# Kernel optimization log

Measured on AMD Instinct MI355X. Metric: run time of the kernel, lower is better.

The kernel has to match this reference:

```python
import jax, jax.numpy as jnp
import numpy as np

PROBE = 1.0
ALPHA = 0.5


def setup_inputs() -> dict:
    key = jax.random.key(0)
    ks = jax.random.split(key, 8)
    B, L, D = 4096, 128, 64  # batch, n_cats (fields), d_embed
    NG, NL = 2, 2
    cat_indices = jax.random.randint(ks[0], (B, L), 0, L, dtype=jnp.int64)
    emb_table = jax.random.normal(ks[1], (L, D), dtype=jnp.float32)
    acc_w = jax.random.normal(ks[2], (D, D), dtype=jnp.float32) * (1.0 / np.sqrt(D))
    acc_b = jnp.zeros((D,), dtype=jnp.float32)
    gw = jax.random.normal(ks[3], (NG, D, D), dtype=jnp.float32) * (1.0 / np.sqrt(D))
    gb = jnp.zeros((NG, D), dtype=jnp.float32)
    lw = jax.random.normal(ks[4], (NL, D, D), dtype=jnp.float32) * (1.0 / np.sqrt(D))
    lb = jnp.zeros((NL, D), dtype=jnp.float32)
    return {"cat_indices": cat_indices, "emb_table": emb_table, "acc_w": acc_w,
            "acc_b": acc_b, "gw": gw, "gb": gb, "lw": lw, "lb": lb}


def reference(cat_indices, emb_table, acc_w, acc_b, gw, gb, lw, lb):
    B, L = cat_indices.shape
    # shallow embedding lookup: [B, L, D]
    emb = emb_table[cat_indices]
    # uniform + probe*I adjacency, row-normalized by (L + probe); identical per sample
    adj = (jnp.ones((L, L), emb.dtype) + PROBE * jnp.eye(L, dtype=emb.dtype)) / (L + PROBE)
    # global branch: adj @ (emb @ W) + b
    support = jnp.einsum('bld,de->ble', emb, acc_w)
    g = jnp.einsum('lm,bme->ble', adj, support) + acc_b
    g = jax.nn.relu(g)
    n_global = gw.shape[0]
    for i in range(n_global):
        g = jnp.einsum('bld,ed->ble', g, gw[i]) + gb[i]
        if i + 1 < n_global:
            g = jax.nn.relu(g)
    # local FM branch: 0.5 * ((sum e)^2 - sum e^2)  -> [B, D]
    s = jnp.sum(emb, axis=1)
    loc = 0.5 * (s * s - jnp.sum(emb * emb, axis=1))
    n_local = lw.shape[0]
    for i in range(n_local):
        loc = loc @ lw[i].T + lb[i]
        if i + 1 < n_local:
            loc = jax.nn.relu(loc)
    # broadcast local [B, D] against global [B, L, D]
    return ALPHA * g + (1.0 - ALPHA) * loc[:, None, :]
```

## Files before the change

kernel.cpp:

```cpp
#include <hip/hip_runtime.h>
#include <hip/hip_bf16.h>


typedef __attribute__((ext_vector_type(8))) short bf16x8;
typedef __attribute__((ext_vector_type(4))) float f32x4;
typedef __attribute__((ext_vector_type(2))) unsigned int u32x2;

#define RECIP129 (1.0f/129.0f)

static __device__ __forceinline__ unsigned int cvt_pk_bf16(float lo, float hi){
  unsigned int r;
  asm("v_cvt_pk_bf16_f32 %0, %1, %2" : "=v"(r) : "v"(lo), "v"(hi));
  return r;
}

__global__ __launch_bounds__(64) void prep_kernel(const float* __restrict__ emb,
                                                  const float* __restrict__ acc_w,
                                                  const float* __restrict__ lw,
                                                  const float* __restrict__ gw,
                                                  unsigned int* __restrict__ tsupb,
                                                  uint4* __restrict__ fragtab){
  const int e = threadIdx.x, blk = blockIdx.x;
  const int r = e & 15, h = e >> 4;
  if (blk < 128){
    float acc = 0.f;
    #pragma unroll
    for (int d = 0; d < 64; ++d) acc += emb[blk*64 + d] * acc_w[d*64 + e];
    acc *= RECIP129;
    float alo = __shfl(acc, 2*(e & 31));
    float ahi = __shfl(acc, 2*(e & 31) + 1);
    if (e < 32) tsupb[blk*32 + e] = cvt_pk_bf16(alo, ahi);
  } else if (blk < 144){
    int f = blk - 128;
    int layer = f >> 3, nt = (f >> 1) & 3, kc = f & 1;
    float sc = layer ? 0.5f : 1.0f;
    const float* p0 = gw + layer*4096 + (nt*16 + r)*64 + kc*32 + h*8;
    float4 a = *reinterpret_cast<const float4*>(p0);
    float4 c = *reinterpret_cast<const float4*>(p0 + 4);
    uint4 v;
    v.x = cvt_pk_bf16(sc*a.x, sc*a.y); v.y = cvt_pk_bf16(sc*a.z, sc*a.w);
    v.z = cvt_pk_bf16(sc*c.x, sc*c.y); v.w = cvt_pk_bf16(sc*c.z, sc*c.w);
    fragtab[f*64 + e] = v;
  } else if (blk < 176){
    int g = blk - 144;
    int sq = g >= 16; if (sq) g -= 16;
    int nt = g >> 2, kc = g & 3;
    const float* base = emb + (kc*32 + h*8)*64 + nt*16 + r;
    unsigned int q[4];
    #pragma unroll
    for (int j2 = 0; j2 < 4; ++j2){
      float x = base[(2*j2)*64], y = base[(2*j2 + 1)*64];
      if (sq){ x *= x; y *= y; }
      q[j2] = cvt_pk_bf16(x, y);
    }
    uint4 v; v.x=q[0]; v.y=q[1]; v.z=q[2]; v.w=q[3];
    fragtab[(16 + sq*16 + g)*64 + e] = v;
  } else if (blk < 184){
    int g = blk - 176;
    int nt = g >> 1, kc = g & 1;
    const float* base = acc_w + (kc*32 + h*8)*64 + nt*16 + r;
    unsigned int q[4];
    #pragma unroll
    for (int j2 = 0; j2 < 4; ++j2)
      q[j2] = cvt_pk_bf16(base[(2*j2)*64]*RECIP129, base[(2*j2+1)*64]*RECIP129);
    uint4 v; v.x=q[0]; v.y=q[1]; v.z=q[2]; v.w=q[3];
    fragtab[(48 + g)*64 + e] = v;
  } else {
    int g = blk - 184;
    int layer = g >> 3, nt = (g >> 1) & 3, kc = g & 1;
    const float* p0 = lw + layer*4096 + (nt*16 + r)*64 + kc*32 + h*8;
    float4 a = *reinterpret_cast<const float4*>(p0);
    float4 c = *reinterpret_cast<const float4*>(p0 + 4);
    uint4 v;
    v.x = cvt_pk_bf16(a.x, a.y); v.y = cvt_pk_bf16(a.z, a.w);
    v.z = cvt_pk_bf16(c.x, c.y); v.w = cvt_pk_bf16(c.z, c.w);
    fragtab[(56 + g)*64 + e] = v;
  }
}

__global__ __launch_bounds__(512) void mega_kernel(
    const int*          __restrict__ cat,
    const unsigned int* __restrict__ tsupb,
    const float*        __restrict__ acc_b,
    const float*        __restrict__ lb,
    const float*        __restrict__ gbias,
    const uint4*        __restrict__ fragtab,
    float*              __restrict__ out)
{
  __shared__ int hist[16*128];
  __shared__ __align__(16) unsigned int  cbf[16*64];
  __shared__ __align__(16) unsigned short srows[16*64];
  __shared__ __align__(16) unsigned short lrows[16*64];
  __shared__ float u_s[16][68];
  __shared__ float l2_s[16][68];
  __shared__ __align__(16) unsigned short ts[128*72];
  __shared__ __align__(16) unsigned short gbuf[8][16*64];

  const int tid = threadIdx.x, w = tid >> 6, lane = tid & 63;
  const int r = lane & 15, h = lane >> 4;
  const int bbase = blockIdx.x * 16;
  const unsigned int swzr = (unsigned)(r & 7) << 4;

  bf16x8 w0[4][2], w1[4][2];
  #pragma unroll
  for (int nt = 0; nt < 4; ++nt)
    #pragma unroll
    for (int kc = 0; kc < 2; ++kc){
      w0[nt][kc] = __builtin_bit_cast(bf16x8, fragtab[(nt*2 + kc)*64 + lane]);
      w1[nt][kc] = __builtin_bit_cast(bf16x8, fragtab[(8 + nt*2 + kc)*64 + lane]);
    }
  f32x4 gb0f[4];
  #pragma unroll
  for (int mt = 0; mt < 4; ++mt){
    float4 gv = *reinterpret_cast<const float4*>(gbias + mt*16 + h*4);
    f32x4 g; g[0]=gv.x; g[1]=gv.y; g[2]=gv.z; g[3]=gv.w;
    gb0f[mt] = g;
  }

  bf16x8 af_s[4], af_q[4], aw[2], l0f[2], l1f[2];
  float accb[4], lb0v[4], bias05[4];
  f32x4 acc_h = {0,0,0,0};
  if (w < 4){
    #pragma unroll
    for (int kc = 0; kc < 4; ++kc){
      af_s[kc] = __builtin_bit_cast(bf16x8, fragtab[(16 + w*4 + kc)*64 + lane]);
      af_q[kc] = __builtin_bit_cast(bf16x8, fragtab[(32 + w*4 + kc)*64 + lane]);
    }
    #pragma unroll
    for (int kc = 0; kc < 2; ++kc){
      aw[kc]  = __builtin_bit_cast(bf16x8, fragtab[(48 + w*2 + kc)*64 + lane]);
      l0f[kc] = __builtin_bit_cast(bf16x8, fragtab[(56 + w*2 + kc)*64 + lane]);
      l1f[kc] = __builtin_bit_cast(bf16x8, fragtab[(64 + w*2 + kc)*64 + lane]);
    }
    const int n = w*16 + h*4;
    #pragma unroll
    for (int reg = 0; reg < 4; ++reg){
      accb[reg]   = acc_b[n + reg];
      lb0v[reg]   = lb[n + reg];
      bias05[reg] = 0.5f*(lb[64 + n + reg] + gbias[64 + n + reg]);
    }
  }

  #pragma unroll
  for (int i = 0; i < 4; ++i) hist[tid*4 + i] = 0;
  __syncthreads();

  if (w < 4){
    int b_l = tid >> 4, l0 = (tid & 15) * 8;
    const int* cp = cat + (bbase + b_l)*128 + l0;
    int4 i0 = *reinterpret_cast<const int4*>(cp);
    int4 i1 = *reinterpret_cast<const int4*>(cp + 4);
    atomicAdd(&hist[b_l*128 + i0.x], 1); atomicAdd(&hist[b_l*128 + i0.y], 1);
    atomicAdd(&hist[b_l*128 + i0.z], 1); atomicAdd(&hist[b_l*128 + i0.w], 1);
    atomicAdd(&hist[b_l*128 + i1.x], 1); atomicAdd(&hist[b_l*128 + i1.y], 1);
    atomicAdd(&hist[b_l*128 + i1.z], 1); atomicAdd(&hist[b_l*128 + i1.w], 1);
  } else {
    int t2 = tid - 256;
    int k = t2 >> 1, half = t2 & 1;
    const uint4* src = reinterpret_cast<const uint4*>(tsupb) + k*8 + half*4;
    char* rowp = (char*)&ts[k*72];
    unsigned int swz = (unsigned)(k & 3) << 4;
    #pragma unroll
    for (int i = 0; i < 4; ++i)
      *reinterpret_cast<uint4*>(rowp + ((unsigned)(half*64 + i*16) ^ swz)) = src[i];
  }
  __syncthreads();

  if (w < 4){
    int b_l = tid >> 4, c0 = (tid & 15) * 8;
    float f[8];
    #pragma unroll
    for (int i = 0; i < 8; ++i) f[i] = (float)hist[b_l*128 + c0 + i];
    uint4 v;
    v.x = cvt_pk_bf16(f[0], f[1]); v.y = cvt_pk_bf16(f[2], f[3]);
    v.z = cvt_pk_bf16(f[4], f[5]); v.w = cvt_pk_bf16(f[6], f[7]);
    *reinterpret_cast<uint4*>((char*)cbf + b_l*256 + ((unsigned)(c0*2) ^ ((unsigned)(b_l & 7) << 4))) = v;
  }
  __syncthreads();

  if (w < 4){
    const char* crow = (const char*)cbf + r*256;
    f32x4 acc_s = {0,0,0,0}, acc_q = {0,0,0,0};
    #pragma unroll
    for (int kc = 0; kc < 4; ++kc){
      bf16x8 cf = __builtin_bit_cast(bf16x8,
          *reinterpret_cast<const uint4*>(crow + ((unsigned)(kc*64 + h*16) ^ swzr)));
      acc_s = __builtin_amdgcn_mfma_f32_16x16x32_bf16(af_s[kc], cf, acc_s, 0, 0, 0);
      acc_q = __builtin_amdgcn_mfma_f32_16x16x32_bf16(af_q[kc], cf, acc_q, 0, 0, 0);
    }
    char* srow = (char*)srows + r*128;
    char* lrow = (char*)lrows + r*128;
    const unsigned int off = ((unsigned)(w*32 + h*8)) ^ swzr;
    u32x2 ps, pl;
    ps[0] = cvt_pk_bf16(acc_s[0], acc_s[1]);
    ps[1] = cvt_pk_bf16(acc_s[2], acc_s[3]);
    float l0 = 0.5f*(acc_s[0]*acc_s[0] - acc_q[0]);
    float l1 = 0.5f*(acc_s[1]*acc_s[1] - acc_q[1]);
    float l2v = 0.5f*(acc_s[2]*acc_s[2] - acc_q[2]);
    float l3 = 0.5f*(acc_s[3]*acc_s[3] - acc_q[3]);
    pl[0] = cvt_pk_bf16(l0, l1); pl[1] = cvt_pk_bf16(l2v, l3);
    *reinterpret_cast<u32x2*>(srow + off) = ps;
    *reinterpret_cast<u32x2*>(lrow + off) = pl;
  }
  __syncthreads();

  if (w < 4){
    f32x4 acc_u; acc_u[0]=accb[0]; acc_u[1]=accb[1]; acc_u[2]=accb[2]; acc_u[3]=accb[3];
    #pragma unroll
    for (int kc = 0; kc < 2; ++kc){
      unsigned o = ((unsigned)(kc*64 + h*16)) ^ swzr;
      bf16x8 sb = __builtin_bit_cast(bf16x8, *reinterpret_cast<const uint4*>((char*)srows + r*128 + o));
      bf16x8 lf = __builtin_bit_cast(bf16x8, *reinterpret_cast<const uint4*>((char*)lrows + r*128 + o));
      acc_u = __builtin_amdgcn_mfma_f32_16x16x32_bf16(aw[kc],  sb, acc_u, 0, 0, 0);
      acc_h = __builtin_amdgcn_mfma_f32_16x16x32_bf16(l0f[kc], lf, acc_h, 0, 0, 0);
    }
    f32x4 st; st[0]=acc_u[0]; st[1]=acc_u[1]; st[2]=acc_u[2]; st[3]=acc_u[3];
    *reinterpret_cast<f32x4*>(&u_s[r][w*16 + h*4]) = st;
  }
  __syncthreads();
  if (w < 4){
    char* lrow = (char*)lrows + r*128;
    const unsigned int off = ((unsigned)(w*32 + h*8)) ^ swzr;
    u32x2 ph;
    ph[0] = cvt_pk_bf16(fmaxf(acc_h[0] + lb0v[0], 0.f), fmaxf(acc_h[1] + lb0v[1], 0.f));
    ph[1] = cvt_pk_bf16(fmaxf(acc_h[2] + lb0v[2], 0.f), fmaxf(acc_h[3] + lb0v[3], 0.f));
    *reinterpret_cast<u32x2*>(lrow + off) = ph;
  }
  __syncthreads();

  if (w < 4){
    f32x4 acc2 = {0,0,0,0};
    #pragma unroll
    for (int kc = 0; kc < 2; ++kc){
      unsigned o = ((unsigned)(kc*64 + h*16)) ^ swzr;
      bf16x8 hf = __builtin_bit_cast(bf16x8, *reinterpret_cast<const uint4*>((char*)lrows + r*128 + o));
      acc2 = __builtin_amdgcn_mfma_f32_16x16x32_bf16(l1f[kc], hf, acc2, 0, 0, 0);
    }
    f32x4 st;
    st[0] = 0.5f*acc2[0] + bias05[0]; st[1] = 0.5f*acc2[1] + bias05[1];
    st[2] = 0.5f*acc2[2] + bias05[2]; st[3] = 0.5f*acc2[3] + bias05[3];
    *reinterpret_cast<f32x4*>(&l2_s[r][w*16 + h*4]) = st;
  }
  __syncthreads();

  char* myrowW = (char*)&gbuf[w][0] + r*128;
  const unsigned int rsw8 = (unsigned)(r & 7) << 4;

  for (int bi = 0; bi < 2; ++bi){
    const int b_l = w*2 + bi;
    const int b = bbase + b_l;
    int ki0 = cat[b*128 + lane];
    int ki1 = cat[b*128 + 64 + lane];

    float uf[16];
    #pragma unroll
    for (int kc = 0; kc < 2; ++kc)
      #pragma unroll
      for (int j = 0; j < 8; ++j)
        uf[kc*8 + j] = u_s[b_l][kc*32 + h*8 + j];

    f32x4 c2i[4];
    #pragma unroll
    for (int mt = 0; mt < 4; ++mt){
      f32x4 t;
      t[0] = l2_s[b_l][mt*16 + h*4 + 0]; t[1] = l2_s[b_l][mt*16 + h*4 + 1];
      t[2] = l2_s[b_l][mt*16 + h*4 + 2]; t[3] = l2_s[b_l][mt*16 + h*4 + 3];
      c2i[mt] = t;
    }

    for (int tl = 0; tl < 8; ++tl){
      const int rowbase = b*128 + tl*16;
      int kk = __shfl(tl < 4 ? ki0 : ki1, (tl & 3)*16 + r);

      const char* trow = (const char*)&ts[kk*72];
      const unsigned int ksw = (unsigned)(kk & 3) << 4;
      bf16x8 a0[2];
      #pragma unroll
      for (int kc = 0; kc < 2; ++kc){
        uint4 wv = *reinterpret_cast<const uint4*>(trow + ((unsigned)(kc*64 + h*16) ^ ksw));
        unsigned int ow[4];
        const unsigned int* wp = &wv.x;
        #pragma unroll
        for (int q = 0; q < 4; ++q){
          unsigned int wq = wp[q];
          float lo = fmaxf(__uint_as_float(wq << 16)         + uf[kc*8 + 2*q],     0.f);
          float hi = fmaxf(__uint_as_float(wq & 0xffff0000u) + uf[kc*8 + 2*q + 1], 0.f);
          ow[q] = cvt_pk_bf16(lo, hi);
        }
        uint4 packed; packed.x=ow[0]; packed.y=ow[1]; packed.z=ow[2]; packed.w=ow[3];
        a0[kc] = __builtin_bit_cast(bf16x8, packed);
      }

      f32x4 acc1[4];
      #pragma unroll
      for (int nt = 0; nt < 4; ++nt) acc1[nt] = gb0f[nt];
      #pragma unroll
      for (int kc = 0; kc < 2; ++kc)
        #pragma unroll
        for (int nt = 0; nt < 4; ++nt)
          acc1[nt] = __builtin_amdgcn_mfma_f32_16x16x32_bf16(w0[nt][kc], a0[kc], acc1[nt], 0, 0, 0);

      #pragma unroll
      for (int nt = 0; nt < 4; ++nt){
        u32x2 p;
        p[0] = cvt_pk_bf16(fmaxf(acc1[nt][0], 0.f), fmaxf(acc1[nt][1], 0.f));
        p[1] = cvt_pk_bf16(fmaxf(acc1[nt][2], 0.f), fmaxf(acc1[nt][3], 0.f));
        *reinterpret_cast<u32x2*>(myrowW + ((unsigned)(nt*32 + h*8) ^ rsw8)) = p;
      }

      bf16x8 a1[2];
      #pragma unroll
      for (int kc = 0; kc < 2; ++kc)
        a1[kc] = __builtin_bit_cast(bf16x8,
                   *reinterpret_cast<const uint4*>(myrowW + ((unsigned)(kc*64 + h*16) ^ rsw8)));

      f32x4 acc2[4];
      #pragma unroll
      for (int mt = 0; mt < 4; ++mt) acc2[mt] = c2i[mt];
      #pragma unroll
      for (int kc = 0; kc < 2; ++kc)
        #pragma unroll
        for (int mt = 0; mt < 4; ++mt)
          acc2[mt] = __builtin_amdgcn_mfma_f32_16x16x32_bf16(w1[mt][kc], a1[kc], acc2[mt], 0, 0, 0);

      float* orow = out + (size_t)(rowbase + r)*64 + h*4;
      #pragma unroll
      for (int mt = 0; mt < 4; ++mt){
        float4 st;
        st.x = acc2[mt][0]; st.y = acc2[mt][1];
        st.z = acc2[mt][2]; st.w = acc2[mt][3];
        *reinterpret_cast<float4*>(orow + mt*16) = st;
      }
    }
  }
}

extern "C" void kernel_launch(void* const* d_in, const int* in_sizes, int n_in,
                              void* d_out, int out_size, void* d_ws, size_t ws_size,
                              hipStream_t stream) {
  const int*   cat   = (const int*)  d_in[0];
  const float* emb   = (const float*)d_in[1];
  const float* acc_w = (const float*)d_in[2];
  const float* acc_b = (const float*)d_in[3];
  const float* gw    = (const float*)d_in[4];
  const float* gb    = (const float*)d_in[5];
  const float* lw    = (const float*)d_in[6];
  const float* lb    = (const float*)d_in[7];
  float* out = (float*)d_out;

  const int B = in_sizes[0] / 128;

  float* ws           = (float*)d_ws;
  unsigned int* tsupb = (unsigned int*)ws;
  uint4* fragtab      = (uint4*)(ws + 4096);

  hipLaunchKernelGGL(prep_kernel, dim3(200), dim3(64), 0, stream,
                     emb, acc_w, lw, gw, tsupb, fragtab);
  hipLaunchKernelGGL(mega_kernel, dim3(B/16), dim3(512), 0, stream,
                     cat, tsupb, acc_b, lb, gb, fragtab, out);
}
```

Before: 37.00 us.

## Halve batch rows per block, add occupancy hint, defer weight loads, nontemporal stores

Each block now handles 8 samples instead of 16, so the grid doubles and each wave processes a single sample instead of looping over two. The histogram build is restructured so every wave reads its own indices once, reusing them for both the atomics and the main loop. The table copy into shared memory is spread across all threads and overlaps with the histogram zeroing, which removes one barrier. Global-branch weight fragments are loaded only after the local phase, to cut register pressure alongside the __launch_bounds__(512,3) hint. Output writes use nontemporal stores. The trade-off is that prep work per block (shared table copy, local MFMAs computed on padded 16-row tiles) is now amortized over half as many samples.

```diff
diff --git a/kernel.cpp b/kernel.cpp
--- a/kernel.cpp
+++ b/kernel.cpp
@@ -78,7 +78,7 @@
   }
 }
 
-__global__ __launch_bounds__(512) void mega_kernel(
+__global__ __launch_bounds__(512, 3) void mega_kernel(
     const int*          __restrict__ cat,
     const unsigned int* __restrict__ tsupb,
     const float*        __restrict__ acc_b,
@@ -87,35 +87,32 @@
     const uint4*        __restrict__ fragtab,
     float*              __restrict__ out)
 {
-  __shared__ int hist[16*128];
+  __shared__ int hist[8*128];
   __shared__ __align__(16) unsigned int  cbf[16*64];
   __shared__ __align__(16) unsigned short srows[16*64];
   __shared__ __align__(16) unsigned short lrows[16*64];
-  __shared__ float u_s[16][68];
-  __shared__ float l2_s[16][68];
+  __shared__ float u_s[8][68];
+  __shared__ float l2_s[8][68];
   __shared__ __align__(16) unsigned short ts[128*72];
   __shared__ __align__(16) unsigned short gbuf[8][16*64];
 
   const int tid = threadIdx.x, w = tid >> 6, lane = tid & 63;
   const int r = lane & 15, h = lane >> 4;
-  const int bbase = blockIdx.x * 16;
+  const int bbase = blockIdx.x * 8;
   const unsigned int swzr = (unsigned)(r & 7) << 4;
 
-  bf16x8 w0[4][2], w1[4][2];
-  #pragma unroll
-  for (int nt = 0; nt < 4; ++nt)
-    #pragma unroll
-    for (int kc = 0; kc < 2; ++kc){
-      w0[nt][kc] = __builtin_bit_cast(bf16x8, fragtab[(nt*2 + kc)*64 + lane]);
-      w1[nt][kc] = __builtin_bit_cast(bf16x8, fragtab[(8 + nt*2 + kc)*64 + lane]);
-    }
-  f32x4 gb0f[4];
-  #pragma unroll
-  for (int mt = 0; mt < 4; ++mt){
-    float4 gv = *reinterpret_cast<const float4*>(gbias + mt*16 + h*4);
-    f32x4 g; g[0]=gv.x; g[1]=gv.y; g[2]=gv.z; g[3]=gv.w;
-    gb0f[mt] = g;
-  }
+  hist[tid] = 0; hist[512 + tid] = 0;
+  {
+    int k = tid >> 2, q = tid & 3;
+    const uint4* src = reinterpret_cast<const uint4*>(tsupb) + k*8 + q*2;
+    char* rowp = (char*)&ts[k*72];
+    unsigned int swz = (unsigned)(k & 3) << 4;
+    *reinterpret_cast<uint4*>(rowp + ((unsigned)(q*32)      ^ swz)) = src[0];
+    *reinterpret_cast<uint4*>(rowp + ((unsigned)(q*32 + 16) ^ swz)) = src[1];
+  }
+  const int b = bbase + w;
+  int ki0 = cat[b*128 + lane];
+  int ki1 = cat[b*128 + 64 + lane];
 
   bf16x8 af_s[4], af_q[4], aw[2], l0f[2], l1f[2];
   float accb[4], lb0v[4], bias05[4];
@@ -140,33 +137,13 @@
       bias05[reg] = 0.5f*(lb[64 + n + reg] + gbias[64 + n + reg]);
     }
   }
-
-  #pragma unroll
-  for (int i = 0; i < 4; ++i) hist[tid*4 + i] = 0;
-  __syncthreads();
-
-  if (w < 4){
-    int b_l = tid >> 4, l0 = (tid & 15) * 8;
-    const int* cp = cat + (bbase + b_l)*128 + l0;
-    int4 i0 = *reinterpret_cast<const int4*>(cp);
-    int4 i1 = *reinterpret_cast<const int4*>(cp + 4);
-    atomicAdd(&hist[b_l*128 + i0.x], 1); atomicAdd(&hist[b_l*128 + i0.y], 1);
-    atomicAdd(&hist[b_l*128 + i0.z], 1); atomicAdd(&hist[b_l*128 + i0.w], 1);
-    atomicAdd(&hist[b_l*128 + i1.x], 1); atomicAdd(&hist[b_l*128 + i1.y], 1);
-    atomicAdd(&hist[b_l*128 + i1.z], 1); atomicAdd(&hist[b_l*128 + i1.w], 1);
-  } else {
-    int t2 = tid - 256;
-    int k = t2 >> 1, half = t2 & 1;
-    const uint4* src = reinterpret_cast<const uint4*>(tsupb) + k*8 + half*4;
-    char* rowp = (char*)&ts[k*72];
-    unsigned int swz = (unsigned)(k & 3) << 4;
-    #pragma unroll
-    for (int i = 0; i < 4; ++i)
-      *reinterpret_cast<uint4*>(rowp + ((unsigned)(half*64 + i*16) ^ swz)) = src[i];
-  }
-  __syncthreads();
-
-  if (w < 4){
+  __syncthreads();
+
+  atomicAdd(&hist[w*128 + ki0], 1);
+  atomicAdd(&hist[w*128 + ki1], 1);
+  __syncthreads();
+
+  if (tid < 128){
     int b_l = tid >> 4, c0 = (tid & 15) * 8;
     float f[8];
     #pragma unroll
@@ -214,8 +191,10 @@
       acc_u = __builtin_amdgcn_mfma_f32_16x16x32_bf16(aw[kc],  sb, acc_u, 0, 0, 0);
       acc_h = __builtin_amdgcn_mfma_f32_16x16x32_bf16(l0f[kc], lf, acc_h, 0, 0, 0);
     }
-    f32x4 st; st[0]=acc_u[0]; st[1]=acc_u[1]; st[2]=acc_u[2]; st[3]=acc_u[3];
-    *reinterpret_cast<f32x4*>(&u_s[r][w*16 + h*4]) = st;
+    if (r < 8){
+      f32x4 st; st[0]=acc_u[0]; st[1]=acc_u[1]; st[2]=acc_u[2]; st[3]=acc_u[3];
+      *reinterpret_cast<f32x4*>(&u_s[r][w*16 + h*4]) = st;
+    }
   }
   __syncthreads();
   if (w < 4){
@@ -236,101 +215,106 @@
       bf16x8 hf = __builtin_bit_cast(bf16x8, *reinterpret_cast<const uint4*>((char*)lrows + r*128 + o));
       acc2 = __builtin_amdgcn_mfma_f32_16x16x32_bf16(l1f[kc], hf, acc2, 0, 0, 0);
     }
-    f32x4 st;
-    st[0] = 0.5f*acc2[0] + bias05[0]; st[1] = 0.5f*acc2[1] + bias05[1];
-    st[2] = 0.5f*acc2[2] + bias05[2]; st[3] = 0.5f*acc2[3] + bias05[3];
-    *reinterpret_cast<f32x4*>(&l2_s[r][w*16 + h*4]) = st;
-  }
-  __syncthreads();
+    if (r < 8){
+      f32x4 st;
+      st[0] = 0.5f*acc2[0] + bias05[0]; st[1] = 0.5f*acc2[1] + bias05[1];
+      st[2] = 0.5f*acc2[2] + bias05[2]; st[3] = 0.5f*acc2[3] + bias05[3];
+      *reinterpret_cast<f32x4*>(&l2_s[r][w*16 + h*4]) = st;
+    }
+  }
+  __syncthreads();
+
+  bf16x8 w0[4][2], w1[4][2];
+  #pragma unroll
+  for (int nt = 0; nt < 4; ++nt)
+    #pragma unroll
+    for (int kc = 0; kc < 2; ++kc){
+      w0[nt][kc] = __builtin_bit_cast(bf16x8, fragtab[(nt*2 + kc)*64 + lane]);
+      w1[nt][kc] = __builtin_bit_cast(bf16x8, fragtab[(8 + nt*2 + kc)*64 + lane]);
+    }
+  f32x4 gb0f[4], c2i[4];
+  #pragma unroll
+  for (int mt = 0; mt < 4; ++mt){
+    float4 gv = *reinterpret_cast<const float4*>(gbias + mt*16 + h*4);
+    f32x4 g; g[0]=gv.x; g[1]=gv.y; g[2]=gv.z; g[3]=gv.w;
+    gb0f[mt] = g;
+    f32x4 t;
+    t[0] = l2_s[w][mt*16 + h*4 + 0]; t[1] = l2_s[w][mt*16 + h*4 + 1];
+    t[2] = l2_s[w][mt*16 + h*4 + 2]; t[3] = l2_s[w][mt*16 + h*4 + 3];
+    c2i[mt] = t;
+  }
+  float uf[16];
+  #pragma unroll
+  for (int kc = 0; kc < 2; ++kc)
+    #pragma unroll
+    for (int j = 0; j < 8; ++j)
+      uf[kc*8 + j] = u_s[w][kc*32 + h*8 + j];
 
   char* myrowW = (char*)&gbuf[w][0] + r*128;
   const unsigned int rsw8 = (unsigned)(r & 7) << 4;
 
-  for (int bi = 0; bi < 2; ++bi){
-    const int b_l = w*2 + bi;
-    const int b = bbase + b_l;
-    int ki0 = cat[b*128 + lane];
-    int ki1 = cat[b*128 + 64 + lane];
-
-    float uf[16];
+  for (int tl = 0; tl < 8; ++tl){
+    const int rowbase = b*128 + tl*16;
+    int kk = __shfl(tl < 4 ? ki0 : ki1, (tl & 3)*16 + r);
+
+    const char* trow = (const char*)&ts[kk*72];
+    const unsigned int ksw = (unsigned)(kk & 3) << 4;
+    bf16x8 a0[2];
+    #pragma unroll
+    for (int kc = 0; kc < 2; ++kc){
+      uint4 wv = *reinterpret_cast<const uint4*>(trow + ((unsigned)(kc*64 + h*16) ^ ksw));
+      unsigned int ow[4];
+      const unsigned int* wp = &wv.x;
+      #pragma unroll
+      for (int q = 0; q < 4; ++q){
+        unsigned int wq = wp[q];
+        float lo = fmaxf(__uint_as_float(wq << 16)         + uf[kc*8 + 2*q],     0.f);
+        float hi = fmaxf(__uint_as_float(wq & 0xffff0000u) + uf[kc*8 + 2*q + 1], 0.f);
+        ow[q] = cvt_pk_bf16(lo, hi);
+      }
+      uint4 packed; packed.x=ow[0]; packed.y=ow[1]; packed.z=ow[2]; packed.w=ow[3];
+      a0[kc] = __builtin_bit_cast(bf16x8, packed);
+    }
+
+    f32x4 acc1[4];
+    #pragma unroll
+    for (int nt = 0; nt < 4; ++nt) acc1[nt] = gb0f[nt];
     #pragma unroll
     for (int kc = 0; kc < 2; ++kc)
       #pragma unroll
-      for (int j = 0; j < 8; ++j)
-        uf[kc*8 + j] = u_s[b_l][kc*32 + h*8 + j];
-
-    f32x4 c2i[4];
+      for (int nt = 0; nt < 4; ++nt)
+        acc1[nt] = __builtin_amdgcn_mfma_f32_16x16x32_bf16(w0[nt][kc], a0[kc], acc1[nt], 0, 0, 0);
+
+    #pragma unroll
+    for (int nt = 0; nt < 4; ++nt){
+      u32x2 p;
+      p[0] = cvt_pk_bf16(fmaxf(acc1[nt][0], 0.f), fmaxf(acc1[nt][1], 0.f));
+      p[1] = cvt_pk_bf16(fmaxf(acc1[nt][2], 0.f), fmaxf(acc1[nt][3], 0.f));
+      *reinterpret_cast<u32x2*>(myrowW + ((unsigned)(nt*32 + h*8) ^ rsw8)) = p;
+    }
+
+    bf16x8 a1[2];
+    #pragma unroll
+    for (int kc = 0; kc < 2; ++kc)
+      a1[kc] = __builtin_bit_cast(bf16x8,
+                 *reinterpret_cast<const uint4*>(myrowW + ((unsigned)(kc*64 + h*16) ^ rsw8)));
+
+    f32x4 acc2[4];
+    #pragma unroll
+    for (int mt = 0; mt < 4; ++mt) acc2[mt] = c2i[mt];
+    #pragma unroll
+    for (int kc = 0; kc < 2; ++kc)
+      #pragma unroll
+      for (int mt = 0; mt < 4; ++mt)
+        acc2[mt] = __builtin_amdgcn_mfma_f32_16x16x32_bf16(w1[mt][kc], a1[kc], acc2[mt], 0, 0, 0);
+
+    float* orow = out + (size_t)(rowbase + r)*64 + h*4;
     #pragma unroll
     for (int mt = 0; mt < 4; ++mt){
-      f32x4 t;
-      t[0] = l2_s[b_l][mt*16 + h*4 + 0]; t[1] = l2_s[b_l][mt*16 + h*4 + 1];
-      t[2] = l2_s[b_l][mt*16 + h*4 + 2]; t[3] = l2_s[b_l][mt*16 + h*4 + 3];
-      c2i[mt] = t;
-    }
-
-    for (int tl = 0; tl < 8; ++tl){
-      const int rowbase = b*128 + tl*16;
-      int kk = __shfl(tl < 4 ? ki0 : ki1, (tl & 3)*16 + r);
-
-      const char* trow = (const char*)&ts[kk*72];
-      const unsigned int ksw = (unsigned)(kk & 3) << 4;
-      bf16x8 a0[2];
-      #pragma unroll
-      for (int kc = 0; kc < 2; ++kc){
-        uint4 wv = *reinterpret_cast<const uint4*>(trow + ((unsigned)(kc*64 + h*16) ^ ksw));
-        unsigned int ow[4];
-        const unsigned int* wp = &wv.x;
-        #pragma unroll
-        for (int q = 0; q < 4; ++q){
-          unsigned int wq = wp[q];
-          float lo = fmaxf(__uint_as_float(wq << 16)         + uf[kc*8 + 2*q],     0.f);
-          float hi = fmaxf(__uint_as_float(wq & 0xffff0000u) + uf[kc*8 + 2*q + 1], 0.f);
-          ow[q] = cvt_pk_bf16(lo, hi);
-        }
-        uint4 packed; packed.x=ow[0]; packed.y=ow[1]; packed.z=ow[2]; packed.w=ow[3];
-        a0[kc] = __builtin_bit_cast(bf16x8, packed);
-      }
-
-      f32x4 acc1[4];
-      #pragma unroll
-      for (int nt = 0; nt < 4; ++nt) acc1[nt] = gb0f[nt];
-      #pragma unroll
-      for (int kc = 0; kc < 2; ++kc)
-        #pragma unroll
-        for (int nt = 0; nt < 4; ++nt)
-          acc1[nt] = __builtin_amdgcn_mfma_f32_16x16x32_bf16(w0[nt][kc], a0[kc], acc1[nt], 0, 0, 0);
-
-      #pragma unroll
-      for (int nt = 0; nt < 4; ++nt){
-        u32x2 p;
-        p[0] = cvt_pk_bf16(fmaxf(acc1[nt][0], 0.f), fmaxf(acc1[nt][1], 0.f));
-        p[1] = cvt_pk_bf16(fmaxf(acc1[nt][2], 0.f), fmaxf(acc1[nt][3], 0.f));
-        *reinterpret_cast<u32x2*>(myrowW + ((unsigned)(nt*32 + h*8) ^ rsw8)) = p;
-      }
-
-      bf16x8 a1[2];
-      #pragma unroll
-      for (int kc = 0; kc < 2; ++kc)
-        a1[kc] = __builtin_bit_cast(bf16x8,
-                   *reinterpret_cast<const uint4*>(myrowW + ((unsigned)(kc*64 + h*16) ^ rsw8)));
-
-      f32x4 acc2[4];
-      #pragma unroll
-      for (int mt = 0; mt < 4; ++mt) acc2[mt] = c2i[mt];
-      #pragma unroll
-      for (int kc = 0; kc < 2; ++kc)
-        #pragma unroll
-        for (int mt = 0; mt < 4; ++mt)
-          acc2[mt] = __builtin_amdgcn_mfma_f32_16x16x32_bf16(w1[mt][kc], a1[kc], acc2[mt], 0, 0, 0);
-
-      float* orow = out + (size_t)(rowbase + r)*64 + h*4;
-      #pragma unroll
-      for (int mt = 0; mt < 4; ++mt){
-        float4 st;
-        st.x = acc2[mt][0]; st.y = acc2[mt][1];
-        st.z = acc2[mt][2]; st.w = acc2[mt][3];
-        *reinterpret_cast<float4*>(orow + mt*16) = st;
-      }
+      f32x4 st;
+      st[0] = acc2[mt][0]; st[1] = acc2[mt][1];
+      st[2] = acc2[mt][2]; st[3] = acc2[mt][3];
+      __builtin_nontemporal_store(st, reinterpret_cast<f32x4*>(orow + mt*16));
     }
   }
 }
@@ -356,6 +340,6 @@
 
   hipLaunchKernelGGL(prep_kernel, dim3(200), dim3(64), 0, stream,
                      emb, acc_w, lw, gw, tsupb, fragtab);
-  hipLaunchKernelGGL(mega_kernel, dim3(B/16), dim3(512), 0, stream,
+  hipLaunchKernelGGL(mega_kernel, dim3(B/8), dim3(512), 0, stream,
                      cat, tsupb, acc_b, lb, gb, fragtab, out);
 }
```

Result: slower. 49.08 us (+32.7%).
